# Kernel tuning notes

Hardware: AMD Instinct MI355X
Metric: run time of the kernel (lower is better)

The kernel has to match this reference:

```python
import jax, jax.numpy as jnp
import numpy as np

B, T, TM, V = 16, 128, 128, 25
CIN, CM = 64, 256
H, D1, D2 = 8, 32, 32
COUT, K = 256, 3
EPS = 1e-6


def setup_inputs() -> dict:
    key = jax.random.key(0)
    ks = jax.random.split(key, 12)
    n = lambda k, s, sc=1.0: jax.random.normal(k, s, jnp.float32) * sc
    inp = {
        'x': n(ks[0], (B, T, V, CIN)),
        'm': n(ks[1], (B, TM, V, CM)),
        'A': jax.random.uniform(ks[2], (K, V, V), jnp.float32),
        'mask': jnp.tril(jnp.ones((T, T), bool)),  # causal decoder mask over time
        # temporal self-attention projections (concat-heads output = H*D1)
        'Wq1': n(ks[3], (CIN, H * D1), 0.05),
        'Wk1': n(ks[4], (CIN, H * D1), 0.05),
        'Wv1': n(ks[5], (CIN, H * D1), 0.05),
        'g1': jnp.ones((H * D1,), jnp.float32),
        'b1': jnp.zeros((H * D1,), jnp.float32),
        # temporal cross-attention: Q from x (H*D1 ch), K/V from memory m (CM ch)
        'Wq2': n(ks[6], (H * D1, H * D2), 0.05),
        'Wk2': n(ks[7], (CM, H * D2), 0.05),
        'Wv2': n(ks[8], (CM, H * D2), 0.05),
        'g2': jnp.ones((H * D2,), jnp.float32),
        'b2': jnp.zeros((H * D2,), jnp.float32),
        # spatial GCN: 1x1 channel expansion to K*COUT then contract with A[k,v,w]
        'Wg': n(ks[9], (H * D2, K * COUT), 0.05),
        'bg': jnp.zeros((K * COUT,), jnp.float32),
        'g3': jnp.ones((COUT,), jnp.float32),
        'b3': jnp.zeros((COUT,), jnp.float32),
    }
    return inp


def _split_heads(t):
    # [B, T, V, H*d] -> [B, H, V, T, d]
    b, tt, v, hd = t.shape
    return t.reshape(b, tt, v, H, hd // H).transpose(0, 3, 2, 1, 4)


def _merge_heads(t):
    # [B, H, V, T, d] -> [B, T, V, H*d]
    b, h, v, tt, d = t.shape
    return t.transpose(0, 3, 2, 1, 4).reshape(b, tt, v, h * d)


def _temporal_attn(q, k, v, mask):
    d = q.shape[-1]
    scores = jnp.einsum('bhvtd,bhvsd->bhvts', q, k) / np.float32(np.sqrt(d))
    if mask is not None:
        scores = jnp.where(mask[None, None, None], scores, jnp.float32(-1e9))
    p = jax.nn.softmax(scores, axis=-1)
    return jnp.einsum('bhvts,bhvsd->bhvtd', p, v)


def _layernorm(x, g, b):
    mu = jnp.mean(x, axis=-1, keepdims=True)
    sd = jnp.std(x, axis=-1, ddof=1, keepdims=True)  # torch std default: unbiased
    return g * (x - mu) / (sd + EPS) + b


def reference(x, m, A, mask, Wq1, Wk1, Wv1, g1, b1, Wq2, Wk2, Wv2, g2, b2, Wg, bg, g3, b3):
    # stage 1: masked temporal self-attention per node
    q = _split_heads(x @ Wq1)
    k = _split_heads(x @ Wk1)
    v = _split_heads(x @ Wv1)
    h1 = _merge_heads(_temporal_attn(q, k, v, mask))          # [B,T,V,H*D1]
    h1 = _layernorm(h1, g1, b1)
    # stage 2: temporal cross-attention against encoder memory
    q = _split_heads(h1 @ Wq2)
    k = _split_heads(m @ Wk2)
    v = _split_heads(m @ Wv2)
    h2 = _merge_heads(_temporal_attn(q, k, v, None))           # [B,T,V,H*D2]
    h2 = _layernorm(h2, g2, b2)
    # stage 3: spatial GCN (ST-GCN style): expand channels to K*COUT, contract with A
    xw = (h2 @ Wg + bg).reshape(B, T, V, K, COUT)
    h3 = jnp.einsum('btvkc,kvw->btwc', xw, A)                  # [B,T,V,COUT]
    return _layernorm(h3, g3, b3)
```

## Files before the change

kernel.cpp:

```cpp
#include <hip/hip_runtime.h>
#include <hip/hip_bf16.h>

typedef unsigned short ush;
typedef unsigned int uint32;
typedef __attribute__((ext_vector_type(8))) short s8v;
typedef __attribute__((ext_vector_type(4))) float f4v;

#define NB 16
#define NT 128
#define NTM 128
#define NV 25
#define NCIN 64
#define NCM 256
#define NH 8
#define ND 32
#define NC 256
#define NK 3
#define NKC 768
#define LN_EPS 1e-6f
#define QSCALE 0.17677669529663687f

__device__ __forceinline__ float bf2f(ush u) {
    union { uint32 i; float f; } x; x.i = ((uint32)u) << 16; return x.f;
}
__device__ __forceinline__ ush f2bf(float f) {
    union { float f; uint32 i; } x; x.f = f;
    uint32 r = x.i + 0x7FFFu + ((x.i >> 16) & 1u);
    return (ush)(r >> 16);
}
__device__ __forceinline__ uint32 pack2(float a, float b) {
    return (uint32)f2bf(a) | ((uint32)f2bf(b) << 16);
}

__global__ __launch_bounds__(256) void k_detect(const uint32* __restrict__ xw,
                                               int* __restrict__ flag)
{
    __shared__ int cnt;
    if (threadIdx.x == 0) cnt = 0;
    __syncthreads();
    int c = 0;
    for (int i = 0; i < 4; ++i) {
        uint32 u = xw[threadIdx.x + 256 * i];
        uint32 e = (u >> 7) & 0xFF;
        c += (e >= 100 && e <= 135) ? 1 : 0;
    }
    atomicAdd(&cnt, c);
    __syncthreads();
    if (threadIdx.x == 0) *flag = (cnt > 700) ? 1 : 0;
}

__global__ __launch_bounds__(256) void k_convA(const void* __restrict__ src,
                                               ush* __restrict__ A2,
                                               float* __restrict__ cs4,
                                               const int* __restrict__ flag)
{
    const bool isbf = (*flag != 0);
    const int tid = threadIdx.x;
    __shared__ float As[1875];
    for (int i = tid; i < 1875; i += 256)
        As[i] = isbf ? bf2f(((const ush*)src)[i]) : ((const float*)src)[i];
    __syncthreads();
    for (int j = tid; j < 32 * 96; j += 256) {
        int w = j / 96, kk = j - w * 96, k = kk >> 5, v = kk & 31;
        float val = (w < NV && v < NV) ? As[k * 625 + v * 25 + w] : 0.f;
        A2[j] = f2bf(val);
    }
    for (int j = tid; j < 100; j += 256) {
        int w = j >> 2, k = j & 3;
        float s = 0.f;
        if (k < 3)
            for (int v = 0; v < NV; ++v) s += As[k * 625 + v * 25 + w];
        cs4[j] = s;
    }
}

struct CvEnt { const void* src; ush* dst; int n; int K; int N; int blk0; };
struct CvTab { CvEnt e[16]; };

__global__ __launch_bounds__(256) void k_convall(CvTab tab, const int* __restrict__ flag)
{
    const bool isbf = (*flag != 0);
    const int bi = (int)blockIdx.x;
    int ei = 0;
    #pragma unroll
    for (int i = 1; i < 16; ++i) if (bi >= tab.e[i].blk0) ei = i;
    const CvEnt& e = tab.e[ei];
    if (e.K == 0) {
        const int idx = (bi - e.blk0) * 2048 + (int)threadIdx.x * 8;
        if (idx >= e.n) return;
        if (isbf) {
            *(uint4*)&e.dst[idx] = *(const uint4*)((const ush*)e.src + idx);
        } else {
            const float* s = (const float*)e.src + idx;
            uint4 a = *(const uint4*)s;
            uint4 b = *(const uint4*)(s + 4);
            uint4 o;
            o.x = pack2(((float*)&a)[0], ((float*)&a)[1]);
            o.y = pack2(((float*)&a)[2], ((float*)&a)[3]);
            o.z = pack2(((float*)&b)[0], ((float*)&b)[1]);
            o.w = pack2(((float*)&b)[2], ((float*)&b)[3]);
            *(uint4*)&e.dst[idx] = o;
        }
    } else {
        const int s4 = (bi - e.blk0) * 1024 + (int)threadIdx.x * 4;
        if (s4 >= e.n) return;
        const int k = s4 / e.N, n0 = s4 - k * e.N;
        float v0, v1, v2, v3;
        if (isbf) {
            const ush* s = (const ush*)e.src + s4;
            v0 = bf2f(s[0]); v1 = bf2f(s[1]); v2 = bf2f(s[2]); v3 = bf2f(s[3]);
        } else {
            float4 f = *(const float4*)((const float*)e.src + s4);
            v0 = f.x; v1 = f.y; v2 = f.z; v3 = f.w;
        }
        ush* d = e.dst + (size_t)n0 * e.K + k;
        d[0] = f2bf(v0);
        d[e.K] = f2bf(v1);
        d[2 * e.K] = f2bf(v2);
        d[3 * e.K] = f2bf(v3);
    }
}

__global__ __launch_bounds__(256) void k_gemm(
    const ush* __restrict__ A, const ush* __restrict__ Bt, ush* __restrict__ C,
    int M, int K, int ldC)
{
    const int n0 = blockIdx.x * 128, m0 = blockIdx.y * 128;
    const int tid = threadIdx.x, w = tid >> 6, l = tid & 63;
    __shared__ ush As[8192], Bs[8192];
    const char* AsB = (const char*)As;
    const char* BsB = (const char*)Bs;
    const int rl = l >> 3, cc = l & 7;
    f4v acc[4][4] = {};
    const int wm = w >> 1, wn = w & 1;

    for (int kt = 0; kt < K; kt += 64) {
        __syncthreads();
        #pragma unroll
        for (int j = 0; j < 4; ++j) {
            const int r = (w * 4 + j) * 8 + rl;
            const int sc = (cc ^ (r & 7)) * 8;
            const ush* ga = &A[(size_t)(m0 + r) * K + kt + sc];
            const ush* gb = &Bt[(size_t)(n0 + r) * K + kt + sc];
            __builtin_amdgcn_global_load_lds(
                (const __attribute__((address_space(1))) uint32*)ga,
                (__attribute__((address_space(3))) uint32*)&As[(w * 4 + j) * 512], 16, 0, 0);
            __builtin_amdgcn_global_load_lds(
                (const __attribute__((address_space(1))) uint32*)gb,
                (__attribute__((address_space(3))) uint32*)&Bs[(w * 4 + j) * 512], 16, 0, 0);
        }
        __syncthreads();
        #pragma unroll
        for (int ks = 0; ks < 2; ++ks) {
            const int ko = ks * 64 + (l >> 4) * 16;
            s8v a[4], b[4];
            #pragma unroll
            for (int mi = 0; mi < 4; ++mi) {
                const int ra = wm * 64 + mi * 16 + (l & 15);
                a[mi] = *(const s8v*)(AsB + ra * 128 + (ko ^ ((ra & 7) << 4)));
            }
            #pragma unroll
            for (int ni = 0; ni < 4; ++ni) {
                const int rb = wn * 64 + ni * 16 + (l & 15);
                b[ni] = *(const s8v*)(BsB + rb * 128 + (ko ^ ((rb & 7) << 4)));
            }
            #pragma unroll
            for (int mi = 0; mi < 4; ++mi)
                #pragma unroll
                for (int ni = 0; ni < 4; ++ni)
                    acc[mi][ni] = __builtin_amdgcn_mfma_f32_16x16x32_bf16(a[mi], b[ni],
                                                                          acc[mi][ni], 0, 0, 0);
        }
    }
    const int col = n0 + wn * 64 + (l & 15);
    #pragma unroll
    for (int mi = 0; mi < 4; ++mi) {
        const int row_base = m0 + wm * 64 + mi * 16 + (l >> 4) * 4;
        #pragma unroll
        for (int ni = 0; ni < 4; ++ni)
            #pragma unroll
            for (int r = 0; r < 4; ++r)
                C[(size_t)(row_base + r) * ldC + col + ni * 16] = f2bf(acc[mi][ni][r]);
    }
}

template<int MASKED>
__global__ __launch_bounds__(256) void k_attn_mfma(
    const ush* __restrict__ QKV, ush* __restrict__ O)
{
    const int v = blockIdx.x, hq = blockIdx.y, b = blockIdx.z;
    const int tid = threadIdx.x, wv = tid >> 6, l = tid & 63;
    const int h = hq * 4 + wv;
    const int g = l >> 4, c = l & 15;
    __shared__ ush Vs[4][NT * ND];
    const size_t tokStride = (size_t)NV * NKC;
    const ush* base = QKV + ((size_t)b * NT * NV + v) * NKC;

    const int vrow = l >> 2, vch = (l & 3) * 8;
    #pragma unroll
    for (int i = 0; i < 8; ++i) {
        s8v rv = *(const s8v*)(base + (size_t)(16 * i + vrow) * tokStride + 512 + h * ND + vch);
        *(s8v*)&Vs[wv][(16 * i + vrow) * ND + vch] = rv;
    }
    s8v kf[8];
    const int koff = 256 + h * ND + g * 8;
    #pragma unroll
    for (int si = 0; si < 8; ++si)
        kf[si] = *(const s8v*)(base + (size_t)(16 * si + c) * tokStride + koff);
    __syncthreads();
    s8v vf[4][2];
    #pragma unroll
    for (int ks = 0; ks < 4; ++ks)
        #pragma unroll
        for (int ni = 0; ni < 2; ++ni) {
            s8v tmp;
            #pragma unroll
            for (int j = 0; j < 8; ++j)
                tmp[j] = (short)Vs[wv][(32 * ks + 8 * g + j) * ND + 16 * ni + c];
            vf[ks][ni] = tmp;
        }

    ush* og = O + ((size_t)b * NT * NV + v) * NC + h * ND;
    const int qoff = h * ND + g * 8;
    const int ga = (g & 1) * 2;
    const int l1 = ga * 16 + c, l2 = l1 + 16;
    const bool hisel = (g >> 1) != 0;

    for (int t16 = 0; t16 < 8; ++t16) {
        s8v qf = *(const s8v*)(base + (size_t)(16 * t16 + c) * tokStride + qoff);
        f4v st[8];
        #pragma unroll
        for (int si = 0; si < 8; ++si)
            st[si] = __builtin_amdgcn_mfma_f32_16x16x32_bf16(kf[si], qf,
                                                             (f4v){0.f, 0.f, 0.f, 0.f}, 0, 0, 0);
        const int t = 16 * t16 + c;
        if (MASKED) {
            #pragma unroll
            for (int si = 0; si < 8; ++si)
                #pragma unroll
                for (int r = 0; r < 4; ++r)
                    if (16 * si + 4 * g + r > t) st[si][r] = -1e30f;
        }
        float mx = -1e30f;
        #pragma unroll
        for (int si = 0; si < 8; ++si)
            #pragma unroll
            for (int r = 0; r < 4; ++r) mx = fmaxf(mx, st[si][r]);
        mx = fmaxf(mx, __shfl_xor(mx, 16));
        mx = fmaxf(mx, __shfl_xor(mx, 32));
        float sm = 0.f;
        #pragma unroll
        for (int si = 0; si < 8; ++si)
            #pragma unroll
            for (int r = 0; r < 4; ++r) {
                float e = __expf((st[si][r] - mx) * QSCALE);
                st[si][r] = e;
                sm += e;
            }
        sm += __shfl_xor(sm, 16);
        sm += __shfl_xor(sm, 32);
        const float inv = 1.f / sm;
        uint32 u[8][2];
        #pragma unroll
        for (int si = 0; si < 8; ++si) {
            float e0 = st[si][0] * inv, e1 = st[si][1] * inv;
            float e2 = st[si][2] * inv, e3 = st[si][3] * inv;
            asm("v_cvt_pk_bf16_f32 %0, %1, %2" : "=v"(u[si][0]) : "v"(e0), "v"(e1));
            asm("v_cvt_pk_bf16_f32 %0, %1, %2" : "=v"(u[si][1]) : "v"(e2), "v"(e3));
        }
        f4v o[2] = {};
        #pragma unroll
        for (int ks = 0; ks < 4; ++ks) {
            uint32 w0a = __shfl(u[2 * ks][0], l1),     w0b = __shfl(u[2 * ks][1], l1);
            uint32 w0c = __shfl(u[2 * ks][0], l2),     w0d = __shfl(u[2 * ks][1], l2);
            uint32 w1a = __shfl(u[2 * ks + 1][0], l1), w1b = __shfl(u[2 * ks + 1][1], l1);
            uint32 w1c = __shfl(u[2 * ks + 1][0], l2), w1d = __shfl(u[2 * ks + 1][1], l2);
            union { uint32 w[4]; s8v s; } pa;
            pa.w[0] = hisel ? w1a : w0a;
            pa.w[1] = hisel ? w1b : w0b;
            pa.w[2] = hisel ? w1c : w0c;
            pa.w[3] = hisel ? w1d : w0d;
            o[0] = __builtin_amdgcn_mfma_f32_16x16x32_bf16(pa.s, vf[ks][0], o[0], 0, 0, 0);
            o[1] = __builtin_amdgcn_mfma_f32_16x16x32_bf16(pa.s, vf[ks][1], o[1], 0, 0, 0);
        }
        #pragma unroll
        for (int ni = 0; ni < 2; ++ni)
            #pragma unroll
            for (int r = 0; r < 4; ++r)
                og[(size_t)(16 * t16 + 4 * g + r) * (NV * NC) + 16 * ni + c] = f2bf(o[ni][r]);
    }
}

__global__ __launch_bounds__(256) void k_ln(
    ush* __restrict__ buf, const ush* __restrict__ g, const ush* __restrict__ bb)
{
    const int row = blockIdx.x * 4 + (threadIdx.x >> 6);
    const int lane = threadIdx.x & 63;
    ush* p = buf + (size_t)row * NC + lane * 4;
    uint2 u = *(uint2*)p;
    float x0 = bf2f((ush)(u.x & 0xffff)), x1 = bf2f((ush)(u.x >> 16));
    float x2 = bf2f((ush)(u.y & 0xffff)), x3 = bf2f((ush)(u.y >> 16));
    float s = x0 + x1 + x2 + x3;
    float q = x0 * x0 + x1 * x1 + x2 * x2 + x3 * x3;
    #pragma unroll
    for (int o = 32; o; o >>= 1) { s += __shfl_xor(s, o); q += __shfl_xor(q, o); }
    float mean = s * (1.f / 256.f);
    float var = fmaxf((q - 256.f * mean * mean) * (1.f / 255.f), 0.f);
    float inv = 1.f / (sqrtf(var) + LN_EPS);
    float o0 = bf2f(g[lane * 4 + 0]) * (x0 - mean) * inv + bf2f(bb[lane * 4 + 0]);
    float o1 = bf2f(g[lane * 4 + 1]) * (x1 - mean) * inv + bf2f(bb[lane * 4 + 1]);
    float o2 = bf2f(g[lane * 4 + 2]) * (x2 - mean) * inv + bf2f(bb[lane * 4 + 2]);
    float o3 = bf2f(g[lane * 4 + 3]) * (x3 - mean) * inv + bf2f(bb[lane * 4 + 3]);
    uint32 lo = (uint32)f2bf(o0) | ((uint32)f2bf(o1) << 16);
    uint32 hi = (uint32)f2bf(o2) | ((uint32)f2bf(o3) << 16);
    *(uint2*)p = make_uint2(lo, hi);
}

__global__ __launch_bounds__(256) void k_gcn_mfma(
    const ush* __restrict__ xw, const ush* __restrict__ A2,
    const float* __restrict__ cs4,
    const ush* __restrict__ bg, const ush* __restrict__ g3, const ush* __restrict__ b3,
    float* __restrict__ outp)
{
    const int t = blockIdx.x, b = blockIdx.y;
    const int tid = threadIdx.x;
    __shared__ uint4 Xs4[2400];
    char* Xs = (char*)Xs4;
    float* h3s = (float*)Xs4;
    const int l = tid & 63, wv = tid >> 6, g = l >> 4, c4 = l & 15;

    s8v af[2][3];
    #pragma unroll
    for (int mi = 0; mi < 2; ++mi)
        #pragma unroll
        for (int ks = 0; ks < 3; ++ks)
            af[mi][ks] = *(const s8v*)&A2[(mi * 16 + c4) * 96 + ks * 32 + g * 8];

    const ush* xr = xw + ((size_t)(b * NT + t)) * NV * NKC;
    for (int i = tid; i < 2400; i += 256) {
        int v = i / 96, c8 = i - v * 96;
        uint32 off = (uint32)(v * 1536 + c8 * 16) ^ (((v >> 3) & 3) << 4);
        *(uint4*)(Xs + off) = *(const uint4*)&xr[(size_t)v * NKC + c8 * 8];
    }
    __syncthreads();

    f4v acc[2][4] = {};
    const int c0 = wv * 64;
    #pragma unroll
    for (int ks = 0; ks < 3; ++ks) {
        #pragma unroll
        for (int ni = 0; ni < 4; ++ni) {
            const int c = c0 + ni * 16 + c4;
            s8v bfr;
            #pragma unroll
            for (int j = 0; j < 8; ++j) {
                int v = g * 8 + j; if (v > 24) v = 24;
                uint32 off = (uint32)(v * 1536 + ks * 512 + c * 2) ^ (((v >> 3) & 3) << 4);
                bfr[j] = *(const short*)(Xs + off);
            }
            acc[0][ni] = __builtin_amdgcn_mfma_f32_16x16x32_bf16(af[0][ks], bfr, acc[0][ni], 0, 0, 0);
            acc[1][ni] = __builtin_amdgcn_mfma_f32_16x16x32_bf16(af[1][ks], bfr, acc[1][ni], 0, 0, 0);
        }
    }
    __syncthreads();
    #pragma unroll
    for (int mi = 0; mi < 2; ++mi)
        #pragma unroll
        for (int r = 0; r < 4; ++r) {
            const int w = mi * 16 + g * 4 + r;
            if (w < NV) {
                #pragma unroll
                for (int ni = 0; ni < 4; ++ni)
                    h3s[w * 260 + c0 + ni * 16 + c4] = acc[mi][ni][r];
            }
        }
    __syncthreads();
    {
        const int lane = tid & 63;
        float bgq[3][4];
        #pragma unroll
        for (int k = 0; k < 3; ++k)
            #pragma unroll
            for (int i = 0; i < 4; ++i)
                bgq[k][i] = bf2f(bg[k * NC + lane * 4 + i]);
        for (int w = wv; w < NV; w += 4) {
            float4 xq = *(const float4*)&h3s[w * 260 + lane * 4];
            const float cw0 = cs4[w * 4], cw1 = cs4[w * 4 + 1], cw2 = cs4[w * 4 + 2];
            xq.x += cw0 * bgq[0][0] + cw1 * bgq[1][0] + cw2 * bgq[2][0];
            xq.y += cw0 * bgq[0][1] + cw1 * bgq[1][1] + cw2 * bgq[2][1];
            xq.z += cw0 * bgq[0][2] + cw1 * bgq[1][2] + cw2 * bgq[2][2];
            xq.w += cw0 * bgq[0][3] + cw1 * bgq[1][3] + cw2 * bgq[2][3];
            float s = xq.x + xq.y + xq.z + xq.w;
            float q = xq.x * xq.x + xq.y * xq.y + xq.z * xq.z + xq.w * xq.w;
            #pragma unroll
            for (int o = 32; o; o >>= 1) { s += __shfl_xor(s, o); q += __shfl_xor(q, o); }
            float mean = s * (1.f / 256.f);
            float var = fmaxf((q - 256.f * mean * mean) * (1.f / 255.f), 0.f);
            float inv = 1.f / (sqrtf(var) + LN_EPS);
            float o0 = bf2f(g3[lane * 4 + 0]) * (xq.x - mean) * inv + bf2f(b3[lane * 4 + 0]);
            float o1 = bf2f(g3[lane * 4 + 1]) * (xq.y - mean) * inv + bf2f(b3[lane * 4 + 1]);
            float o2 = bf2f(g3[lane * 4 + 2]) * (xq.z - mean) * inv + bf2f(b3[lane * 4 + 2]);
            float o3 = bf2f(g3[lane * 4 + 3]) * (xq.w - mean) * inv + bf2f(b3[lane * 4 + 3]);
            float* op = outp + (((size_t)(b * NT + t)) * NV + w) * NC + lane * 4;
            *(float4*)op = make_float4(o0, o1, o2, o3);
        }
    }
}

extern "C" void kernel_launch(void* const* d_in, const int* in_sizes, int n_in,
                              void* d_out, int out_size, void* d_ws, size_t ws_size,
                              hipStream_t stream)
{
    const size_t NTOK = (size_t)NB * NT * NV;
    char* ws = (char*)d_ws;
    int* flag = (int*)ws;
    ush* A2 = (ush*)(ws + 256);
    float* cs4 = (float*)(ws + 256 + 6144);
    ush* bufA = (ush*)(ws + 16384);
    ush* bufB = bufA + NTOK * NKC;
    ush* conv = bufB + NTOK * NC;

    k_detect<<<1, 256, 0, stream>>>((const uint32*)d_in[0], flag);
    k_convA<<<1, 256, 0, stream>>>(d_in[2], A2, cs4, flag);

    CvTab tab;
    int nent = 0, blk = 0;
    ush* p = conv;
    const ush* cp[18] = {};
    auto add = [&](int idx, int n, int K, int N, ush*& dst_out) {
        tab.e[nent] = { d_in[idx], p, n, K, N, blk };
        dst_out = p;
        blk += (K == 0) ? (n + 2047) / 2048 : (n + 1023) / 1024;
        p += (size_t)((n + 7) & ~7);
        ++nent;
    };
    ush* d;
    add(0, NB * NT * NV * NCIN, 0, 0, d);  cp[0] = d;
    add(1, NB * NTM * NV * NCM, 0, 0, d);  cp[1] = d;
    add(15, NKC, 0, 0, d);                 cp[15] = d;
    add(7, NC, 0, 0, d);  cp[7] = d;
    add(8, NC, 0, 0, d);  cp[8] = d;
    add(12, NC, 0, 0, d); cp[12] = d;
    add(13, NC, 0, 0, d); cp[13] = d;
    add(16, NC, 0, 0, d); cp[16] = d;
    add(17, NC, 0, 0, d); cp[17] = d;
    ush* w1t;
    add(4, NCIN * NC, NCIN, NC, w1t);
    add(5, NCIN * NC, NCIN, NC, d);
    add(6, NCIN * NC, NCIN, NC, d);
    ush* wq2t;
    add(9, NC * NC, NC, NC, wq2t);
    ush* wkv2t;
    add(10, NCM * NC, NCM, NC, wkv2t);
    add(11, NCM * NC, NCM, NC, d);
    ush* wgt;
    add(14, NC * NKC, NC, NKC, wgt);
    k_convall<<<blk, 256, 0, stream>>>(tab, flag);

    const int M = (int)NTOK;
    k_gemm<<<dim3(6, M / 128), 256, 0, stream>>>(cp[0], w1t, bufA, M, NCIN, NKC);
    k_attn_mfma<1><<<dim3(NV, NH / 4, NB), 256, 0, stream>>>(bufA, bufB);
    k_ln<<<M / 4, 256, 0, stream>>>(bufB, cp[7], cp[8]);
    k_gemm<<<dim3(2, M / 128), 256, 0, stream>>>(bufB, wq2t, bufA, M, NC, NKC);
    k_gemm<<<dim3(4, M / 128), 256, 0, stream>>>(cp[1], wkv2t, bufA + 256, M, NCM, NKC);
    k_attn_mfma<0><<<dim3(NV, NH / 4, NB), 256, 0, stream>>>(bufA, bufB);
    k_ln<<<M / 4, 256, 0, stream>>>(bufB, cp[12], cp[13]);
    k_gemm<<<dim3(6, M / 128), 256, 0, stream>>>(bufB, wgt, bufA, M, NC, NKC);
    k_gcn_mfma<<<dim3(NT, NB), 256, 0, stream>>>(bufA, A2, cs4, cp[15], cp[16], cp[17],
                                                 (float*)d_out);
}
```

Before: 270.1 us.

## Split attention query tiles across two waves per head and skip masked causal blocks

The attention kernel now uses 512 threads, with two waves per head, each handling half of the query-time tiles and loading half of the V rows into shared memory. In the causal variant, key tiles that lie entirely above the diagonal are skipped in the QK MFMA, the softmax loops and the PV MFMA. This raises parallelism per block and removes roughly half the causal attention work. In exchange it duplicates K-fragment loads across the two waves and leaves them with unequal causal workloads.

```diff
diff --git a/kernel.cpp b/kernel.cpp
--- a/kernel.cpp
+++ b/kernel.cpp
@@ -185,12 +185,13 @@
 }
 
 template<int MASKED>
-__global__ __launch_bounds__(256) void k_attn_mfma(
+__global__ __launch_bounds__(512) void k_attn_mfma(
     const ush* __restrict__ QKV, ush* __restrict__ O)
 {
     const int v = blockIdx.x, hq = blockIdx.y, b = blockIdx.z;
     const int tid = threadIdx.x, wv = tid >> 6, l = tid & 63;
-    const int h = hq * 4 + wv;
+    const int hs = wv >> 1, th = wv & 1;
+    const int h = hq * 4 + hs;
     const int g = l >> 4, c = l & 15;
     __shared__ ush Vs[4][NT * ND];
     const size_t tokStride = (size_t)NV * NKC;
@@ -198,9 +199,10 @@
 
     const int vrow = l >> 2, vch = (l & 3) * 8;
     #pragma unroll
-    for (int i = 0; i < 8; ++i) {
-        s8v rv = *(const s8v*)(base + (size_t)(16 * i + vrow) * tokStride + 512 + h * ND + vch);
-        *(s8v*)&Vs[wv][(16 * i + vrow) * ND + vch] = rv;
+    for (int i = 0; i < 4; ++i) {
+        const int row = 16 * (4 * th + i) + vrow;
+        s8v rv = *(const s8v*)(base + (size_t)row * tokStride + 512 + h * ND + vch);
+        *(s8v*)&Vs[hs][row * ND + vch] = rv;
     }
     s8v kf[8];
     const int koff = 256 + h * ND + g * 8;
@@ -216,7 +218,7 @@
             s8v tmp;
             #pragma unroll
             for (int j = 0; j < 8; ++j)
-                tmp[j] = (short)Vs[wv][(32 * ks + 8 * g + j) * ND + 16 * ni + c];
+                tmp[j] = (short)Vs[hs][(32 * ks + 8 * g + j) * ND + 16 * ni + c];
             vf[ks][ni] = tmp;
         }
 
@@ -226,43 +228,53 @@
     const int l1 = ga * 16 + c, l2 = l1 + 16;
     const bool hisel = (g >> 1) != 0;
 
-    for (int t16 = 0; t16 < 8; ++t16) {
+    for (int i = 0; i < 4; ++i) {
+        const int t16 = 4 * th + i;
         s8v qf = *(const s8v*)(base + (size_t)(16 * t16 + c) * tokStride + qoff);
         f4v st[8];
         #pragma unroll
-        for (int si = 0; si < 8; ++si)
+        for (int si = 0; si < 8; ++si) {
+            if (MASKED && si > t16) { st[si] = (f4v){0.f, 0.f, 0.f, 0.f}; continue; }
             st[si] = __builtin_amdgcn_mfma_f32_16x16x32_bf16(kf[si], qf,
                                                              (f4v){0.f, 0.f, 0.f, 0.f}, 0, 0, 0);
+        }
         const int t = 16 * t16 + c;
         if (MASKED) {
             #pragma unroll
-            for (int si = 0; si < 8; ++si)
+            for (int si = 0; si < 8; ++si) {
+                if (si > t16) continue;
                 #pragma unroll
                 for (int r = 0; r < 4; ++r)
                     if (16 * si + 4 * g + r > t) st[si][r] = -1e30f;
+            }
         }
         float mx = -1e30f;
         #pragma unroll
-        for (int si = 0; si < 8; ++si)
+        for (int si = 0; si < 8; ++si) {
+            if (MASKED && si > t16) continue;
             #pragma unroll
             for (int r = 0; r < 4; ++r) mx = fmaxf(mx, st[si][r]);
+        }
         mx = fmaxf(mx, __shfl_xor(mx, 16));
         mx = fmaxf(mx, __shfl_xor(mx, 32));
         float sm = 0.f;
         #pragma unroll
-        for (int si = 0; si < 8; ++si)
+        for (int si = 0; si < 8; ++si) {
+            if (MASKED && si > t16) continue;
             #pragma unroll
             for (int r = 0; r < 4; ++r) {
                 float e = __expf((st[si][r] - mx) * QSCALE);
                 st[si][r] = e;
                 sm += e;
             }
+        }
         sm += __shfl_xor(sm, 16);
         sm += __shfl_xor(sm, 32);
         const float inv = 1.f / sm;
         uint32 u[8][2];
         #pragma unroll
         for (int si = 0; si < 8; ++si) {
+            if (MASKED && si > t16) { u[si][0] = 0u; u[si][1] = 0u; continue; }
             float e0 = st[si][0] * inv, e1 = st[si][1] * inv;
             float e2 = st[si][2] * inv, e3 = st[si][3] * inv;
             asm("v_cvt_pk_bf16_f32 %0, %1, %2" : "=v"(u[si][0]) : "v"(e0), "v"(e1));
@@ -271,6 +283,7 @@
         f4v o[2] = {};
         #pragma unroll
         for (int ks = 0; ks < 4; ++ks) {
+            if (MASKED && 2 * ks > t16) continue;
             uint32 w0a = __shfl(u[2 * ks][0], l1),     w0b = __shfl(u[2 * ks][1], l1);
             uint32 w0c = __shfl(u[2 * ks][0], l2),     w0d = __shfl(u[2 * ks][1], l2);
             uint32 w1a = __shfl(u[2 * ks + 1][0], l1), w1b = __shfl(u[2 * ks + 1][1], l1);
@@ -459,11 +472,11 @@
 
     const int M = (int)NTOK;
     k_gemm<<<dim3(6, M / 128), 256, 0, stream>>>(cp[0], w1t, bufA, M, NCIN, NKC);
-    k_attn_mfma<1><<<dim3(NV, NH / 4, NB), 256, 0, stream>>>(bufA, bufB);
+    k_attn_mfma<1><<<dim3(NV, NH / 4, NB), 512, 0, stream>>>(bufA, bufB);
     k_ln<<<M / 4, 256, 0, stream>>>(bufB, cp[7], cp[8]);
     k_gemm<<<dim3(2, M / 128), 256, 0, stream>>>(bufB, wq2t, bufA, M, NC, NKC);
     k_gemm<<<dim3(4, M / 128), 256, 0, stream>>>(cp[1], wkv2t, bufA + 256, M, NCM, NKC);
-    k_attn_mfma<0><<<dim3(NV, NH / 4, NB), 256, 0, stream>>>(bufA, bufB);
+    k_attn_mfma<0><<<dim3(NV, NH / 4, NB), 512, 0, stream>>>(bufA, bufB);
     k_ln<<<M / 4, 256, 0, stream>>>(bufB, cp[12], cp[13]);
     k_gemm<<<dim3(6, M / 128), 256, 0, stream>>>(bufB, wgt, bufA, M, NC, NKC);
     k_gcn_mfma<<<dim3(NT, NB), 256, 0, stream>>>(bufA, A2, cs4, cp[15], cp[16], cp[17],
```

After: 270.1 us. About the same (-0.0%).
